# Kernel optimization log

Measured on AMD Instinct MI355X. Metric: run time of the kernel, lower is better.

The kernel has to match this reference:

```python
import jax, jax.numpy as jnp
import numpy as np

B, P, T, V, H, E, C = 256, 256, 32, 3433, 512, 300, 128


def _gru(x, h, W_ih, W_hh, b_ih, b_hh):
    # torch.nn.GRUCell math (bias=True default)
    gx = x @ W_ih.T + b_ih          # (B, 3H)
    gh = h @ W_hh.T + b_hh          # (B, 3H)
    xr, xz, xn = jnp.split(gx, 3, axis=-1)
    hr, hz, hn = jnp.split(gh, 3, axis=-1)
    r = jax.nn.sigmoid(xr + hr)
    z = jax.nn.sigmoid(xz + hz)
    n = jnp.tanh(xn + r * hn)
    return (1.0 - z) * n + z * h


def setup_inputs() -> dict:
    key = jax.random.key(0)
    ks = jax.random.split(key, 24)
    s = 0.02
    inp = {
        'word_embs': jax.random.normal(ks[0], (B, T, E), jnp.float32),
        't_feat': jax.random.normal(ks[1], (B, C), jnp.float32),
        'c_feats': jax.random.normal(ks[2], (B, P, C), jnp.float32),
        'num_words': T,
        # top-down unit (all Linears bias=False)
        'W_td1': jax.random.normal(ks[3], (128, H), jnp.float32) * s,
        'W_td2': jax.random.normal(ks[4], (128, C), jnp.float32) * s,
        'W_td3': jax.random.normal(ks[5], (128, E), jnp.float32) * s,
        'W_td':  jax.random.normal(ks[6], (128, 128), jnp.float32) * s,
        'W1_ih': jax.random.normal(ks[7], (3 * H, 128), jnp.float32) * s,
        'W1_hh': jax.random.normal(ks[8], (3 * H, H), jnp.float32) * s,
        'b1_ih': jax.random.normal(ks[9], (3 * H,), jnp.float32) * s,
        'b1_hh': jax.random.normal(ks[10], (3 * H,), jnp.float32) * s,
        # additive attention
        'W_feat': jax.random.normal(ks[11], (H, C), jnp.float32) * s,
        'W_hidd': jax.random.normal(ks[12], (H, H), jnp.float32) * s,
        'W_att':  jax.random.normal(ks[13], (1, H), jnp.float32) * s,
        # language unit
        'W_l1': jax.random.normal(ks[14], (128, C), jnp.float32) * s,
        'W_l2': jax.random.normal(ks[15], (128, H), jnp.float32) * s,
        'W_l':  jax.random.normal(ks[16], (128, 128), jnp.float32) * s,
        'W2_ih': jax.random.normal(ks[17], (3 * H, 128), jnp.float32) * s,
        'W2_hh': jax.random.normal(ks[18], (3 * H, H), jnp.float32) * s,
        'b2_ih': jax.random.normal(ks[19], (3 * H,), jnp.float32) * s,
        'b2_hh': jax.random.normal(ks[20], (3 * H,), jnp.float32) * s,
        # classifier (bias=True)
        'W_cls': jax.random.normal(ks[21], (V, H), jnp.float32) * s,
        'b_cls': jax.random.normal(ks[22], (V,), jnp.float32) * s,
    }
    return inp


def reference(word_embs, t_feat, c_feats, num_words,
              W_td1, W_td2, W_td3, W_td, W1_ih, W1_hh, b1_ih, b1_hh,
              W_feat, W_hidd, W_att, W_l1, W_l2, W_l,
              W2_ih, W2_hh, b2_ih, b2_hh, W_cls, b_cls):
    n_steps = num_words - 1  # python int, static
    # precompute attention key projection of proposals: (B, P, H)
    feat_proj = jnp.einsum('bpc,hc->bph', c_feats, W_feat)
    td_t = t_feat @ W_td2.T  # (B, 128), time-invariant

    def step_fn(carry, x_t):
        h1, h2 = carry
        # top-down input
        s = x_t @ W_td3.T + h2 @ W_td1.T + td_t
        s = jax.nn.relu(jnp.tanh(s) @ W_td.T)
        h1 = _gru(s, h1, W1_ih, W1_hh, b1_ih, b1_hh)
        # additive attention over proposals
        comb = jnp.tanh(feat_proj + (h1 @ W_hidd.T)[:, None, :])  # (B, P, H)
        scores = jnp.einsum('bph,h->bp', comb, W_att[0])           # (B, P)
        mask = jax.nn.softmax(scores, axis=1)                      # (B, P)
        attended = jnp.einsum('bpc,bp->bc', c_feats, mask)         # (B, C)
        # language input
        l = jnp.tanh(attended @ W_l1.T + h1 @ W_l2.T)
        l = jax.nn.relu(l @ W_l.T)
        h2 = _gru(l, h2, W2_ih, W2_hh, b2_ih, b2_hh)
        logits = h2 @ W_cls.T + b_cls                              # (B, V)
        return (h1, h2), (logits, mask)

    h0 = (jnp.zeros((word_embs.shape[0], H), word_embs.dtype),
          jnp.zeros((word_embs.shape[0], H), word_embs.dtype))
    xs = jnp.swapaxes(word_embs[:, :n_steps], 0, 1)  # (T-1, B, E)
    _, (logits, masks) = jax.lax.scan(step_fn, h0, xs)
    lang_cap = jnp.swapaxes(logits, 0, 1)            # (B, T-1, V)
    topdown_attn = jnp.transpose(masks, (1, 2, 0))   # (B, P, T-1)
    return lang_cap, topdown_attn
```

## Files before the change

kernel.cpp:

```cpp
#include <hip/hip_runtime.h>
#include <hip/hip_bf16.h>

namespace {

constexpr int kB  = 256;
constexpr int kP  = 256;
constexpr int kT  = 32;
constexpr int kNS = 31;
constexpr int kV  = 3433;
constexpr int kH  = 512;
constexpr int kE  = 300;
constexpr int kC  = 128;
constexpr int kG  = 1536;

typedef __bf16 bf16x8 __attribute__((ext_vector_type(8)));
typedef float f32x4 __attribute__((ext_vector_type(4)));

__device__ __forceinline__ float fexp2(float x) {
  float r; asm("v_exp_f32 %0, %1" : "=v"(r) : "v"(x)); return r;
}
__device__ __forceinline__ float frcp(float x) {
  float r; asm("v_rcp_f32 %0, %1" : "=v"(r) : "v"(x)); return r;
}
__device__ __forceinline__ float ftanh(float x) {
  float e = fexp2(x * 2.8853900817779268f);
  return 1.0f - 2.0f * frcp(e + 1.0f);
}
__device__ __forceinline__ float fsigm(float x) {
  return frcp(1.0f + fexp2(x * -1.4426950408889634f));
}
__device__ __forceinline__ float ptanh(float x) {
  x = fminf(3.0f, fmaxf(-3.0f, x));
  float t = x * x;
  float num = x * fmaf(t, fmaf(t, 378.0f + t, 17325.0f), 135135.0f);
  float den = fmaf(t, fmaf(t, fmaf(t, 28.0f, 3150.0f), 62370.0f), 135135.0f);
  return num * frcp(den);
}
__device__ __forceinline__ unsigned short f2bf(float f) {
  unsigned u = __float_as_uint(f);
  u += 0x7FFFu + ((u >> 16) & 1u);
  return (unsigned short)(u >> 16);
}
__device__ __forceinline__ float bf2f(unsigned short s) {
  return __uint_as_float((unsigned)s << 16);
}
__device__ __forceinline__ bf16x8 bload(const unsigned short* p) {
  union { uint4 u; bf16x8 v; } x;
  x.u = *(const uint4*)p;
  return x.v;
}

__global__ void k_transpose(const float* s0, const float* s1, const float* s2,
                            const float* s3, const float* s4, const float* s5,
                            const float* s6, const float* s7, const float* s8,
                            float* d0, float* d1, float* d2, float* d3,
                            float* d4, float* d5, float* d6, float* d7,
                            float* d8) {
  const float* src; float* dst; int R, Cd;
  switch (blockIdx.y) {
    case 0:  src = s0; dst = d0; R = 128;  Cd = 300; break;
    case 1:  src = s1; dst = d1; R = 128;  Cd = 512; break;
    case 2:  src = s2; dst = d2; R = 128;  Cd = 128; break;
    case 3:  src = s3; dst = d3; R = 128;  Cd = 128; break;
    case 4:  src = s4; dst = d4; R = 128;  Cd = 512; break;
    case 5:  src = s5; dst = d5; R = 128;  Cd = 128; break;
    case 6:  src = s6; dst = d6; R = 1536; Cd = 128; break;
    case 7:  src = s7; dst = d7; R = 1536; Cd = 128; break;
    default: src = s8; dst = d8; R = 512;  Cd = 512; break;
  }
  int n = R * Cd;
  for (int i = blockIdx.x * blockDim.x + threadIdx.x; i < n;
       i += gridDim.x * blockDim.x) {
    int k = i / R, r = i - k * R;
    dst[i] = src[r * Cd + k];
  }
}

__global__ void k_tobf16(const float* s0, const float* s1, const float* s2,
                         const float* s3, const float* s4, const float* s5,
                         const float* s6, const float* s7,
                         unsigned short* d0, unsigned short* d1,
                         unsigned short* d2, unsigned short* d3,
                         unsigned short* d4, unsigned short* d5,
                         unsigned short* d6, unsigned short* d7) {
  const float* s; unsigned short* d; int n;
  switch (blockIdx.y) {
    case 0:  s = s0; d = d0; n = kC * kC; break;
    case 1:  s = s1; d = d1; n = kH * kC; break;
    case 2:  s = s2; d = d2; n = kC * kC; break;
    case 3:  s = s3; d = d3; n = kC * kG; break;
    case 4:  s = s4; d = d4; n = kH * kH; break;
    case 5:  s = s5; d = d5; n = kH * kC; break;
    case 6:  s = s6; d = d6; n = kC * kC; break;
    default: s = s7; d = d7; n = kC * kG; break;
  }
  for (int i = blockIdx.x * blockDim.x + threadIdx.x; i < n;
       i += gridDim.x * blockDim.x)
    d[i] = f2bf(s[i]);
}

__global__ void k_split(const float* s0, const float* s1, const float* s2,
                        const float* s3,
                        unsigned short* h0, unsigned short* l0,
                        unsigned short* h1, unsigned short* l1,
                        unsigned short* h2, unsigned short* l2,
                        unsigned short* h3, unsigned short* l3) {
  const float* s; unsigned short* h; unsigned short* l; int n;
  switch (blockIdx.y) {
    case 0:  s = s0; h = h0; l = l0; n = kG * kH; break;
    case 1:  s = s1; h = h1; l = l1; n = kG * kH; break;
    case 2:  s = s2; h = h2; l = l2; n = kV * kH; break;
    default: s = s3; h = h3; l = l3; n = kH * kC; break;
  }
  for (int i = blockIdx.x * blockDim.x + threadIdx.x; i < n;
       i += gridDim.x * blockDim.x) {
    float v = s[i];
    unsigned short hb = f2bf(v);
    h[i] = hb;
    l[i] = f2bf(v - bf2f(hb));
  }
}

__global__ void k_init(const float* __restrict__ t_feat,
                       const float* __restrict__ W_td2,
                       float* __restrict__ td, float* __restrict__ h1,
                       float* __restrict__ h2,
                       unsigned short* __restrict__ h1h,
                       unsigned short* __restrict__ h1l,
                       unsigned short* __restrict__ h2h,
                       unsigned short* __restrict__ h2l) {
  int tid = blockIdx.x * 256 + threadIdx.x;
  int b = tid >> 7, c = tid & 127;
  const float* tf = t_feat + b * kC;
  const float* w  = W_td2 + c * kC;
  float acc = 0.f;
  for (int k = 0; k < kC; ++k) acc = fmaf(tf[k], w[k], acc);
  td[tid] = acc;
  for (int i = tid; i < kB * kH; i += (1 << 15)) {
    h1[i] = 0.f; h2[i] = 0.f;
    h1h[i] = 0; h1l[i] = 0; h2h[i] = 0; h2l[i] = 0;
  }
}

__global__ __launch_bounds__(256) void k_xw(
    const float* __restrict__ word_embs, const float* __restrict__ td3t,
    const float* __restrict__ td, float* __restrict__ xw) {
  __shared__ float xl[4 * 300];
  __shared__ float tdl[512];
  int t = blockIdx.y, b0 = blockIdx.x * 4, tid = threadIdx.x;
  #pragma unroll
  for (int r = 0; r < 4; ++r) {
    const float* xs = word_embs + (size_t)(b0 + r) * (kT * kE) + (size_t)t * kE;
    for (int e = tid; e < kE; e += 256) xl[r * kE + e] = xs[e];
  }
  for (int i = tid; i < 512; i += 256) tdl[i] = td[(size_t)b0 * kC + i];
  __syncthreads();
  #pragma unroll
  for (int q = 0; q < 2; ++q) {
    int idx = tid + q * 256;
    int r = idx >> 7, c = idx & 127;
    float acc = tdl[idx];
    const float* xr = xl + r * kE;
    const float* w3 = td3t + c;
    for (int e = 0; e < kE; ++e) acc = fmaf(xr[e], w3[(size_t)e * 128], acc);
    xw[((size_t)t * kB + b0 + r) * kC + c] = acc;
  }
}

__global__ __launch_bounds__(256) void k_prestep(
    const float* __restrict__ xw, const unsigned short* __restrict__ tdbt,
    const unsigned short* __restrict__ iht1b, const float* __restrict__ b1_ih,
    float* __restrict__ gx1) {
  __shared__ float s1l[128];
  __shared__ float s2l[128];
  __shared__ float part[256];
  int b = blockIdx.x, tid = threadIdx.x;
  if (tid < 128) s1l[tid] = ftanh(xw[(size_t)b * kC + tid]);
  __syncthreads();
  {
    int c = tid & 127, g = tid >> 7;
    float s = 0.f;
    const unsigned short* w = tdbt + (size_t)(g * 64) * kC + c;
    for (int k = 0; k < 64; ++k)
      s = fmaf(s1l[g * 64 + k], bf2f(w[(size_t)k * kC]), s);
    part[g * 128 + c] = s;
  }
  __syncthreads();
  if (tid < 128) s2l[tid] = fmaxf(part[tid] + part[128 + tid], 0.f);
  __syncthreads();
  #pragma unroll
  for (int q = 0; q < 6; ++q) {
    int j = q * 256 + tid;
    float acc = b1_ih[j];
    const unsigned short* w = iht1b + j;
    for (int k = 0; k < kC; ++k)
      acc = fmaf(s2l[k], bf2f(w[(size_t)k * kG]), acc);
    gx1[(size_t)b * kG + j] = acc;
  }
}

__device__ __forceinline__ void mm_tile_lds(
    const unsigned short* __restrict__ Ah, const unsigned short* __restrict__ Al,
    const unsigned short* __restrict__ Bh, const unsigned short* __restrict__ Bl,
    int m0, int n0, int K, int nMax, f32x4 acc[4][4],
    unsigned short* sAh, unsigned short* sAl,
    unsigned short* sBh, unsigned short* sBl) {
  int tid = threadIdx.x;
  int lane = tid & 63, wid = tid >> 6;
  int wm = (wid >> 1) * 64, wn = (wid & 1) * 64;
  int r16 = lane & 15, kq = lane >> 4;
  int rA = tid >> 2, cA = (tid & 3) * 8;
  int brow0 = n0 + rA;       if (brow0 > nMax) brow0 = nMax;
  int brow1 = n0 + rA + 64;  if (brow1 > nMax) brow1 = nMax;
  for (int k0 = 0; k0 < K; k0 += 32) {
    uint4 va0 = *(const uint4*)(Ah + (size_t)(m0 + rA) * K + k0 + cA);
    uint4 va1 = *(const uint4*)(Ah + (size_t)(m0 + rA + 64) * K + k0 + cA);
    uint4 vb0 = *(const uint4*)(Al + (size_t)(m0 + rA) * K + k0 + cA);
    uint4 vb1 = *(const uint4*)(Al + (size_t)(m0 + rA + 64) * K + k0 + cA);
    uint4 vc0 = *(const uint4*)(Bh + (size_t)brow0 * K + k0 + cA);
    uint4 vc1 = *(const uint4*)(Bh + (size_t)brow1 * K + k0 + cA);
    uint4 vd0 = *(const uint4*)(Bl + (size_t)brow0 * K + k0 + cA);
    uint4 vd1 = *(const uint4*)(Bl + (size_t)brow1 * K + k0 + cA);
    __syncthreads();
    *(uint4*)&sAh[rA * 32 + cA] = va0;
    *(uint4*)&sAh[(rA + 64) * 32 + cA] = va1;
    *(uint4*)&sAl[rA * 32 + cA] = vb0;
    *(uint4*)&sAl[(rA + 64) * 32 + cA] = vb1;
    *(uint4*)&sBh[rA * 32 + cA] = vc0;
    *(uint4*)&sBh[(rA + 64) * 32 + cA] = vc1;
    *(uint4*)&sBl[rA * 32 + cA] = vd0;
    *(uint4*)&sBl[(rA + 64) * 32 + cA] = vd1;
    __syncthreads();
    bf16x8 ah[4], al[4], bh[4], bl[4];
    #pragma unroll
    for (int i = 0; i < 4; ++i) {
      int ar = (wm + i * 16 + r16) * 32 + kq * 8;
      int br = (wn + i * 16 + r16) * 32 + kq * 8;
      ah[i] = *(const bf16x8*)&sAh[ar];
      al[i] = *(const bf16x8*)&sAl[ar];
      bh[i] = *(const bf16x8*)&sBh[br];
      bl[i] = *(const bf16x8*)&sBl[br];
    }
    #pragma unroll
    for (int i = 0; i < 4; ++i)
      #pragma unroll
      for (int j = 0; j < 4; ++j) {
        acc[i][j] = __builtin_amdgcn_mfma_f32_16x16x32_bf16(ah[i], bh[j], acc[i][j], 0, 0, 0);
        acc[i][j] = __builtin_amdgcn_mfma_f32_16x16x32_bf16(ah[i], bl[j], acc[i][j], 0, 0, 0);
        acc[i][j] = __builtin_amdgcn_mfma_f32_16x16x32_bf16(al[i], bh[j], acc[i][j], 0, 0, 0);
      }
  }
}

__global__ __launch_bounds__(256) void k_featproj(
    const float* __restrict__ A, const unsigned short* __restrict__ Wh,
    const unsigned short* __restrict__ Wl, unsigned short* __restrict__ out) {
  int lane = threadIdx.x & 63, wid = threadIdx.x >> 6;
  int wm = (wid >> 1) * 64, wn = (wid & 1) * 64;
  int r16 = lane & 15, kq = lane >> 4;
  int m0 = blockIdx.x * 128, n0 = blockIdx.y * 128;
  f32x4 acc[4][4];
  #pragma unroll
  for (int i = 0; i < 4; ++i)
    #pragma unroll
    for (int j = 0; j < 4; ++j) acc[i][j] = (f32x4){0.f, 0.f, 0.f, 0.f};
  for (int k0 = 0; k0 < kC; k0 += 32) {
    int kk = k0 + kq * 8;
    bf16x8 ah[4], al[4], bh[4], bl[4];
    #pragma unroll
    for (int i = 0; i < 4; ++i) {
      const float* pa = A + (size_t)(m0 + wm + i * 16 + r16) * kC + kk;
      float4 v0 = *(const float4*)pa;
      float4 v1 = *(const float4*)(pa + 4);
      float vv[8] = {v0.x, v0.y, v0.z, v0.w, v1.x, v1.y, v1.z, v1.w};
      union { unsigned short s[8]; bf16x8 v; } uh, ul;
      #pragma unroll
      for (int q = 0; q < 8; ++q) {
        unsigned short hb = f2bf(vv[q]);
        uh.s[q] = hb;
        ul.s[q] = f2bf(vv[q] - bf2f(hb));
      }
      ah[i] = uh.v; al[i] = ul.v;
      const unsigned short* pb = Wh + (size_t)(n0 + wn + i * 16 + r16) * kC + kk;
      const unsigned short* pl = Wl + (size_t)(n0 + wn + i * 16 + r16) * kC + kk;
      bh[i] = bload(pb); bl[i] = bload(pl);
    }
    #pragma unroll
    for (int i = 0; i < 4; ++i)
      #pragma unroll
      for (int j = 0; j < 4; ++j) {
        acc[i][j] = __builtin_amdgcn_mfma_f32_16x16x32_bf16(ah[i], bh[j], acc[i][j], 0, 0, 0);
        acc[i][j] = __builtin_amdgcn_mfma_f32_16x16x32_bf16(ah[i], bl[j], acc[i][j], 0, 0, 0);
        acc[i][j] = __builtin_amdgcn_mfma_f32_16x16x32_bf16(al[i], bh[j], acc[i][j], 0, 0, 0);
      }
  }
  #pragma unroll
  for (int i = 0; i < 4; ++i)
    #pragma unroll
    for (int j = 0; j < 4; ++j)
      #pragma unroll
      for (int r = 0; r < 4; ++r) {
        int m = m0 + wm + i * 16 + kq * 4 + r;
        int n = n0 + wn + j * 16 + r16;
        out[(size_t)m * kH + n] = f2bf(acc[i][j][r]);
      }
}

__global__ __launch_bounds__(256) void k_gh(
    const unsigned short* __restrict__ h1h, const unsigned short* __restrict__ h1l,
    const unsigned short* __restrict__ h2h, const unsigned short* __restrict__ h2l,
    const unsigned short* __restrict__ w1hh_h, const unsigned short* __restrict__ w1hh_l,
    const unsigned short* __restrict__ w2hh_h, const unsigned short* __restrict__ w2hh_l,
    const float* __restrict__ b1_hh, const float* __restrict__ b2_hh,
    float* __restrict__ gh1, float* __restrict__ gh2) {
  __shared__ __align__(16) unsigned short sAh[4096], sAl[4096], sBh[4096], sBl[4096];
  int g = blockIdx.x;
  const unsigned short *Ah, *Al, *Wh, *Wl; const float* bias; float* out;
  if (g < 24) { Ah = h1h; Al = h1l; Wh = w1hh_h; Wl = w1hh_l;
                bias = b1_hh; out = gh1; }
  else { g -= 24; Ah = h2h; Al = h2l; Wh = w2hh_h; Wl = w2hh_l;
         bias = b2_hh; out = gh2; }
  int m0 = (g / 12) * 128, n0 = (g % 12) * 128;
  f32x4 acc[4][4];
  #pragma unroll
  for (int i = 0; i < 4; ++i)
    #pragma unroll
    for (int j = 0; j < 4; ++j) acc[i][j] = (f32x4){0.f, 0.f, 0.f, 0.f};
  mm_tile_lds(Ah, Al, Wh, Wl, m0, n0, kH, kG - 1, acc, sAh, sAl, sBh, sBl);
  int tid = threadIdx.x;
  int lane = tid & 63, wid = tid >> 6;
  int wm = (wid >> 1) * 64, wn = (wid & 1) * 64;
  int r16 = lane & 15, kq = lane >> 4;
  #pragma unroll
  for (int i = 0; i < 4; ++i)
    #pragma unroll
    for (int j = 0; j < 4; ++j)
      #pragma unroll
      for (int r = 0; r < 4; ++r) {
        int m = m0 + wm + i * 16 + kq * 4 + r;
        int n = n0 + wn + j * 16 + r16;
        out[(size_t)m * kG + n] = acc[i][j][r] + bias[n];
      }
}

__global__ __launch_bounds__(1024, 4) void k_step2(
    float* __restrict__ gx1, const float* __restrict__ gh1,
    const float* __restrict__ gh2,
    float* __restrict__ h1, float* __restrict__ h2,
    unsigned short* __restrict__ h1h, unsigned short* __restrict__ h1l,
    unsigned short* __restrict__ h2h, unsigned short* __restrict__ h2l,
    const unsigned short* __restrict__ whdbT, const float* __restrict__ W_att,
    const unsigned short* __restrict__ fp, const float* __restrict__ c_feats,
    const unsigned short* __restrict__ l1bt, const unsigned short* __restrict__ l2bt,
    const unsigned short* __restrict__ lbt, const unsigned short* __restrict__ iht2b,
    const float* __restrict__ b2_ih,
    const unsigned short* __restrict__ td1bt, const unsigned short* __restrict__ tdbt,
    const unsigned short* __restrict__ iht1b, const float* __restrict__ b1_ih,
    const float* __restrict__ xw,
    unsigned short* __restrict__ h2all_h, unsigned short* __restrict__ h2all_l,
    float* __restrict__ mask_ws, int t) {
  __shared__ float partbuf[8192];
  __shared__ float h1p[512];
  __shared__ float h2p[512];
  __shared__ float hqs[512];
  __shared__ float scs[256];
  __shared__ float red[16];
  __shared__ float red2[16];
  __shared__ float attl[128];
  __shared__ float lt1[128];
  __shared__ float llv[128];
  __shared__ float s1l[128];
  __shared__ float s2l[128];
  __shared__ float gx2l[1536];
  const int b = blockIdx.x;
  const int tid = threadIdx.x;
  const int lane = tid & 63, wv = tid >> 6;

  if (tid < 512) {
    int c = tid;
    float gr = gx1[(size_t)b * kG + c];
    float gz = gx1[(size_t)b * kG + 512 + c];
    float gn = gx1[(size_t)b * kG + 1024 + c];
    float hr = gh1[(size_t)b * kG + c];
    float hz = gh1[(size_t)b * kG + 512 + c];
    float hnv = gh1[(size_t)b * kG + 1024 + c];
    float rr = fsigm(gr + hr);
    float zz = fsigm(gz + hz);
    float nn = ftanh(gn + rr * hnv);
    float ho = h1[(size_t)b * kH + c];
    float hn = (1.f - zz) * nn + zz * ho;
    h1[(size_t)b * kH + c] = hn;
    h1p[c] = hn;
    unsigned short hb = f2bf(hn);
    h1h[(size_t)b * kH + c] = hb;
    h1l[(size_t)b * kH + c] = f2bf(hn - bf2f(hb));
  }
  __syncthreads();

  {
    int cg = tid & 63, kg = tid >> 6;
    int c0 = cg * 8;
    const unsigned short* w = whdbT + (size_t)(kg * 32) * kH + c0;
    float acc[8] = {};
    #pragma unroll 4
    for (int k = 0; k < 32; ++k) {
      union { uint4 u; unsigned short s[8]; } wu;
      wu.u = *(const uint4*)(w + (size_t)k * kH);
      float h = h1p[kg * 32 + k];
      #pragma unroll
      for (int j = 0; j < 8; ++j) acc[j] = fmaf(h, bf2f(wu.s[j]), acc[j]);
    }
    float* pp = &partbuf[kg * 512 + c0];
    #pragma unroll
    for (int j = 0; j < 8; ++j) pp[j] = acc[j];
  }
  __syncthreads();
  if (tid < 512) {
    float s = 0.f;
    #pragma unroll
    for (int g = 0; g < 16; ++g) s += partbuf[g * 512 + tid];
    hqs[tid] = s;
  }
  __syncthreads();

  {
    float hq8[8], aw[8];
    #pragma unroll
    for (int j = 0; j < 8; ++j) hq8[j] = hqs[lane * 8 + j];
    {
      float4 a0 = *(const float4*)(W_att + lane * 8);
      float4 a1 = *(const float4*)(W_att + lane * 8 + 4);
      aw[0] = a0.x; aw[1] = a0.y; aw[2] = a0.z; aw[3] = a0.w;
      aw[4] = a1.x; aw[5] = a1.y; aw[6] = a1.z; aw[7] = a1.w;
    }
    const unsigned short* fpb = fp + (size_t)b * kP * kH;
    int p0 = wv * 16;
    uint4 rv = *(const uint4*)(fpb + (size_t)p0 * kH + lane * 8);
    for (int p = p0; p < p0 + 16; ++p) {
      union { uint4 v; unsigned short s[8]; } u; u.v = rv;
      if (p + 1 < p0 + 16)
        rv = *(const uint4*)(fpb + (size_t)(p + 1) * kH + lane * 8);
      float sc = 0.f;
      #pragma unroll
      for (int j = 0; j < 8; ++j) {
        float f = __uint_as_float((unsigned)u.s[j] << 16);
        sc += aw[j] * ptanh(f + hq8[j]);
      }
      #pragma unroll
      for (int m = 32; m; m >>= 1) sc += __shfl_xor(sc, m, 64);
      if (lane == 0) scs[p] = sc;
    }
  }
  __syncthreads();

  {
    float sv = (tid < 256) ? scs[tid] : -1e30f;
    float mx = sv;
    #pragma unroll
    for (int m = 32; m; m >>= 1) mx = fmaxf(mx, __shfl_xor(mx, m, 64));
    if (lane == 0) red[wv] = mx;
    __syncthreads();
    float bm = red[0];
    #pragma unroll
    for (int i = 1; i < 16; ++i) bm = fmaxf(bm, red[i]);
    float ev = (tid < 256) ? fexp2((sv - bm) * 1.4426950408889634f) : 0.f;
    float sm = ev;
    #pragma unroll
    for (int m = 32; m; m >>= 1) sm += __shfl_xor(sm, m, 64);
    if (lane == 0) red2[wv] = sm;
    __syncthreads();
    float tot = 0.f;
    #pragma unroll
    for (int i = 0; i < 16; ++i) tot += red2[i];
    if (tid < 256) {
      float mk = ev * frcp(tot);
      scs[tid] = mk;
      mask_ws[(size_t)t * (kB * kP) + (size_t)b * kP + tid] = mk;
    }
  }
  __syncthreads();

  {
    int c = tid & 127, q = tid >> 7;
    const float* cf = c_feats + ((size_t)b * kP + q * 32) * kC + c;
    const float* ms = scs + q * 32;
    float acc = 0.f;
    for (int p = 0; p < 32; ++p) acc = fmaf(ms[p], cf[(size_t)p * kC], acc);
    partbuf[q * 128 + c] = acc;
  }
  __syncthreads();
  if (tid < 128) {
    float s = 0.f;
    #pragma unroll
    for (int q = 0; q < 8; ++q) s += partbuf[q * 128 + tid];
    attl[tid] = s;
  }
  __syncthreads();

  {
    if (tid < 512) {
      int cg = tid & 15, kg = tid >> 4;
      int c0 = cg * 8;
      const unsigned short* w = l2bt + (size_t)(kg * 16) * kC + c0;
      float acc[8] = {};
      for (int k = 0; k < 16; ++k) {
        union { uint4 u; unsigned short s[8]; } wu;
        wu.u = *(const uint4*)(w + (size_t)k * kC);
        float h = h1p[kg * 16 + k];
        #pragma unroll
        for (int j = 0; j < 8; ++j) acc[j] = fmaf(h, bf2f(wu.s[j]), acc[j]);
      }
      float* pp = &partbuf[kg * 128 + c0];
      #pragma unroll
      for (int j = 0; j < 8; ++j) pp[j] = acc[j];
    } else if (tid < 768) {
      int tt = tid - 512;
      int cg = tt & 15, kg = tt >> 4;
      int c0 = cg * 8;
      const unsigned short* w = l1bt + (size_t)(kg * 8) * kC + c0;
      float acc[8] = {};
      for (int k = 0; k < 8; ++k) {
        union { uint4 u; unsigned short s[8]; } wu;
        wu.u = *(const uint4*)(w + (size_t)k * kC);
        float a = attl[kg * 8 + k];
        #pragma unroll
        for (int j = 0; j < 8; ++j) acc[j] = fmaf(a, bf2f(wu.s[j]), acc[j]);
      }
      float* pp = &partbuf[4096 + kg * 128 + c0];
      #pragma unroll
      for (int j = 0; j < 8; ++j) pp[j] = acc[j];
    }
  }
  __syncthreads();
  if (tid < 128) {
    float s = 0.f;
    #pragma unroll
    for (int g = 0; g < 32; ++g) s += partbuf[g * 128 + tid];
    #pragma unroll
    for (int g = 0; g < 16; ++g) s += partbuf[4096 + g * 128 + tid];
    lt1[tid] = ftanh(s);
  }
  __syncthreads();

  if (tid < 256) {
    int cg = tid & 15, kg = tid >> 4;
    int c0 = cg * 8;
    const unsigned short* w = lbt + (size_t)(kg * 8) * kC + c0;
    float acc[8] = {};
    for (int k = 0; k < 8; ++k) {
      union { uint4 u; unsigned short s[8]; } wu;
      wu.u = *(const uint4*)(w + (size_t)k * kC);
      float l = lt1[kg * 8 + k];
      #pragma unroll
      for (int j = 0; j < 8; ++j) acc[j] = fmaf(l, bf2f(wu.s[j]), acc[j]);
    }
    float* pp = &partbuf[kg * 128 + c0];
    #pragma unroll
    for (int j = 0; j < 8; ++j) pp[j] = acc[j];
  }
  __syncthreads();
  if (tid < 128) {
    float s = 0.f;
    #pragma unroll
    for (int g = 0; g < 16; ++g) s += partbuf[g * 128 + tid];
    llv[tid] = fmaxf(s, 0.f);
  }
  __syncthreads();

  if (tid < 768) {
    int cg = tid % 192, kg = tid / 192;
    int c0 = cg * 8;
    const unsigned short* w = iht2b + (size_t)(kg * 32) * kG + c0;
    float acc[8] = {};
    #pragma unroll 4
    for (int k = 0; k < 32; ++k) {
      union { uint4 u; unsigned short s[8]; } wu;
      wu.u = *(const uint4*)(w + (size_t)k * kG);
      float l = llv[kg * 32 + k];
      #pragma unroll
      for (int j = 0; j < 8; ++j) acc[j] = fmaf(l, bf2f(wu.s[j]), acc[j]);
    }
    float* pp = &partbuf[kg * 1536 + c0];
    #pragma unroll
    for (int j = 0; j < 8; ++j) pp[j] = acc[j];
  }
  __syncthreads();
  for (int c = tid; c < kG; c += 1024) {
    float s = b2_ih[c];
    #pragma unroll
    for (int g = 0; g < 4; ++g) s += partbuf[g * 1536 + c];
    gx2l[c] = s;
  }
  __syncthreads();
  if (tid < 512) {
    int c = tid;
    float ghr = gh2[(size_t)b * kG + c];
    float ghz = gh2[(size_t)b * kG + 512 + c];
    float ghn = gh2[(size_t)b * kG + 1024 + c];
    float rr = fsigm(gx2l[c] + ghr);
    float zz = fsigm(gx2l[512 + c] + ghz);
    float nn = ftanh(gx2l[1024 + c] + rr * ghn);
    float ho = h2[(size_t)b * kH + c];
    float hn = (1.f - zz) * nn + zz * ho;
    h2[(size_t)b * kH + c] = hn;
    h2p[c] = hn;
    unsigned short hb = f2bf(hn);
    unsigned short lb = f2bf(hn - bf2f(hb));
    h2h[(size_t)b * kH + c] = hb;
    h2l[(size_t)b * kH + c] = lb;
    size_t o = ((size_t)t * kB + b) * kH + c;
    h2all_h[o] = hb;
    h2all_l[o] = lb;
  }
  __syncthreads();

  if (t + 1 < kNS) {
    if (tid < 512) {
      int cg = tid & 15, kg = tid >> 4;
      int c0 = cg * 8;
      const unsigned short* w = td1bt + (size_t)(kg * 16) * kC + c0;
      float acc[8] = {};
      for (int k = 0; k < 16; ++k) {
        union { uint4 u; unsigned short s[8]; } wu;
        wu.u = *(const uint4*)(w + (size_t)k * kC);
        float h = h2p[kg * 16 + k];
        #pragma unroll
        for (int j = 0; j < 8; ++j) acc[j] = fmaf(h, bf2f(wu.s[j]), acc[j]);
      }
      float* pp = &partbuf[kg * 128 + c0];
      #pragma unroll
      for (int j = 0; j < 8; ++j) pp[j] = acc[j];
    }
    __syncthreads();
    if (tid < 128) {
      float s = xw[((size_t)(t + 1) * kB + b) * kC + tid];
      #pragma unroll
      for (int g = 0; g < 32; ++g) s += partbuf[g * 128 + tid];
      s1l[tid] = ftanh(s);
    }
    __syncthreads();
    if (tid < 256) {
      int cg = tid & 15, kg = tid >> 4;
      int c0 = cg * 8;
      const unsigned short* w = tdbt + (size_t)(kg * 8) * kC + c0;
      float acc[8] = {};
      for (int k = 0; k < 8; ++k) {
        union { uint4 u; unsigned short s[8]; } wu;
        wu.u = *(const uint4*)(w + (size_t)k * kC);
        float sv = s1l[kg * 8 + k];
        #pragma unroll
        for (int j = 0; j < 8; ++j) acc[j] = fmaf(sv, bf2f(wu.s[j]), acc[j]);
      }
      float* pp = &partbuf[kg * 128 + c0];
      #pragma unroll
      for (int j = 0; j < 8; ++j) pp[j] = acc[j];
    }
    __syncthreads();
    if (tid < 128) {
      float s = 0.f;
      #pragma unroll
      for (int g = 0; g < 16; ++g) s += partbuf[g * 128 + tid];
      s2l[tid] = fmaxf(s, 0.f);
    }
    __syncthreads();
    if (tid < 768) {
      int cg = tid % 192, kg = tid / 192;
      int c0 = cg * 8;
      const unsigned short* w = iht1b + (size_t)(kg * 32) * kG + c0;
      float acc[8] = {};
      #pragma unroll 4
      for (int k = 0; k < 32; ++k) {
        union { uint4 u; unsigned short s[8]; } wu;
        wu.u = *(const uint4*)(w + (size_t)k * kG);
        float sv = s2l[kg * 32 + k];
        #pragma unroll
        for (int j = 0; j < 8; ++j) acc[j] = fmaf(sv, bf2f(wu.s[j]), acc[j]);
      }
      float* pp = &partbuf[kg * 1536 + c0];
      #pragma unroll
      for (int j = 0; j < 8; ++j) pp[j] = acc[j];
    }
    __syncthreads();
    for (int c = tid; c < kG; c += 1024) {
      float s = b1_ih[c];
      #pragma unroll
      for (int g = 0; g < 4; ++g) s += partbuf[g * 1536 + c];
      gx1[(size_t)b * kG + c] = s;
    }
  }
}

__global__ __launch_bounds__(256) void k_atrans(
    const float* __restrict__ mws, float* __restrict__ attn_out) {
  int pair = blockIdx.x * 256 + threadIdx.x;
  #pragma unroll
  for (int t = 0; t < kNS; ++t)
    attn_out[(size_t)pair * kNS + t] = mws[(size_t)t * (kB * kP) + pair];
}

__global__ __launch_bounds__(256) void k_cls(
    const unsigned short* __restrict__ Ah, const unsigned short* __restrict__ Al,
    const unsigned short* __restrict__ Wh, const unsigned short* __restrict__ Wl,
    const float* __restrict__ bc, float* __restrict__ out) {
  __shared__ __align__(16) unsigned short sAh[4096], sAl[4096], sBh[4096], sBl[4096];
  int m0 = blockIdx.x * 128, n0 = blockIdx.y * 128;
  f32x4 acc[4][4];
  #pragma unroll
  for (int i = 0; i < 4; ++i)
    #pragma unroll
    for (int j = 0; j < 4; ++j) acc[i][j] = (f32x4){0.f, 0.f, 0.f, 0.f};
  mm_tile_lds(Ah, Al, Wh, Wl, m0, n0, kH, kV - 1, acc, sAh, sAl, sBh, sBl);
  int lane = threadIdx.x & 63, wid = threadIdx.x >> 6;
  int wm = (wid >> 1) * 64, wn = (wid & 1) * 64;
  int r16 = lane & 15, kq = lane >> 4;
  #pragma unroll
  for (int i = 0; i < 4; ++i)
    #pragma unroll
    for (int j = 0; j < 4; ++j)
      #pragma unroll
      for (int r = 0; r < 4; ++r) {
        int m = m0 + wm + i * 16 + kq * 4 + r;
        int n = n0 + wn + j * 16 + r16;
        if (n < kV) {
          int tt = m >> 8, b = m & 255;
          out[(size_t)b * (kNS * kV) + (size_t)tt * kV + n] = acc[i][j][r] + bc[n];
        }
      }
}

}

extern "C" void kernel_launch(void* const* d_in, const int* in_sizes, int n_in,
                              void* d_out, int out_size, void* d_ws,
                              size_t ws_size, hipStream_t stream) {
  (void)in_sizes; (void)n_in; (void)out_size; (void)ws_size;
  const float* word_embs = (const float*)d_in[0];
  const float* t_feat    = (const float*)d_in[1];
  const float* c_feats   = (const float*)d_in[2];
  const float* W_td1 = (const float*)d_in[4];
  const float* W_td2 = (const float*)d_in[5];
  const float* W_td3 = (const float*)d_in[6];
  const float* W_td  = (const float*)d_in[7];
  const float* W1_ih = (const float*)d_in[8];
  const float* W1_hh = (const float*)d_in[9];
  const float* b1_ih = (const float*)d_in[10];
  const float* b1_hh = (const float*)d_in[11];
  const float* W_feat = (const float*)d_in[12];
  const float* W_hidd = (const float*)d_in[13];
  const float* W_att  = (const float*)d_in[14];
  const float* W_l1 = (const float*)d_in[15];
  const float* W_l2 = (const float*)d_in[16];
  const float* W_l  = (const float*)d_in[17];
  const float* W2_ih = (const float*)d_in[18];
  const float* W2_hh = (const float*)d_in[19];
  const float* b2_ih = (const float*)d_in[20];
  const float* b2_hh = (const float*)d_in[21];
  const float* W_cls = (const float*)d_in[22];
  const float* b_cls = (const float*)d_in[23];

  float* lang = (float*)d_out;
  float* attn_out = lang + (size_t)kB * kNS * kV;
  unsigned short* fp = (unsigned short*)d_out;

  float* p = (float*)d_ws;
  float* h1 = p;      p += kB * kH;
  float* h2 = p;      p += kB * kH;
  float* td = p;      p += kB * kC;
  float* gx1 = p;     p += (size_t)kB * kG;
  float* gh1 = p;     p += (size_t)kB * kG;
  float* gh2 = p;     p += (size_t)kB * kG;
  float* mask_ws = p; p += (size_t)kNS * kB * kP;
  float* xw = p;      p += (size_t)kNS * kB * kC;
  float* td3t = p;    p += kE * 128;
  float* td1t = p;    p += kH * 128;
  float* tdt  = p;    p += 128 * 128;
  float* l1t  = p;    p += 128 * 128;
  float* l2t  = p;    p += kH * 128;
  float* lt   = p;    p += 128 * 128;
  float* iht1 = p;    p += 128 * kG;
  float* iht2 = p;    p += 128 * kG;
  float* whd_t = p;   p += kH * kH;

  unsigned short* u = (unsigned short*)p;
  unsigned short* h1h = u;     u += kB * kH;
  unsigned short* h1l = u;     u += kB * kH;
  unsigned short* h2h = u;     u += kB * kH;
  unsigned short* h2l = u;     u += kB * kH;
  unsigned short* w1hh_h = u;  u += (size_t)kG * kH;
  unsigned short* w1hh_l = u;  u += (size_t)kG * kH;
  unsigned short* w2hh_h = u;  u += (size_t)kG * kH;
  unsigned short* w2hh_l = u;  u += (size_t)kG * kH;
  unsigned short* wc_h = u;    u += (size_t)kV * kH;
  unsigned short* wc_l = u;    u += (size_t)kV * kH;
  unsigned short* wf_h = u;    u += (size_t)kH * kC;
  unsigned short* wf_l = u;    u += (size_t)kH * kC;
  unsigned short* h2all_h = u; u += (size_t)kNS * kB * kH;
  unsigned short* h2all_l = u; u += (size_t)kNS * kB * kH;
  unsigned short* l1bt = u;    u += kC * kC;
  unsigned short* l2bt = u;    u += (size_t)kH * kC;
  unsigned short* lbt = u;     u += kC * kC;
  unsigned short* iht2b = u;   u += (size_t)kC * kG;
  unsigned short* whdbT = u;   u += (size_t)kH * kH;
  unsigned short* td1bt = u;   u += (size_t)kH * kC;
  unsigned short* tdbt = u;    u += kC * kC;
  unsigned short* iht1b = u;   u += (size_t)kC * kG;

  k_transpose<<<dim3(64, 9), 256, 0, stream>>>(
      W_td3, W_td1, W_td, W_l1, W_l2, W_l, W1_ih, W2_ih, W_hidd,
      td3t, td1t, tdt, l1t, l2t, lt, iht1, iht2, whd_t);
  k_tobf16<<<dim3(96, 8), 256, 0, stream>>>(
      l1t, l2t, lt, iht2, whd_t, td1t, tdt, iht1,
      l1bt, l2bt, lbt, iht2b, whdbT, td1bt, tdbt, iht1b);
  k_split<<<dim3(256, 4), 256, 0, stream>>>(
      W1_hh, W2_hh, W_cls, W_feat,
      w1hh_h, w1hh_l, w2hh_h, w2hh_l, wc_h, wc_l, wf_h, wf_l);
  k_init<<<128, 256, 0, stream>>>(t_feat, W_td2, td, h1, h2,
                                  h1h, h1l, h2h, h2l);
  k_featproj<<<dim3(512, 4), 256, 0, stream>>>(c_feats, wf_h, wf_l, fp);
  k_xw<<<dim3(64, kNS), 256, 0, stream>>>(word_embs, td3t, td, xw);
  k_prestep<<<256, 256, 0, stream>>>(xw, tdbt, iht1b, b1_ih, gx1);

  for (int t = 0; t < kNS; ++t) {
    k_gh<<<48, 256, 0, stream>>>(h1h, h1l, h2h, h2l,
                                 w1hh_h, w1hh_l, w2hh_h, w2hh_l,
                                 b1_hh, b2_hh, gh1, gh2);
    k_step2<<<256, 1024, 0, stream>>>(gx1, gh1, gh2, h1, h2,
                                      h1h, h1l, h2h, h2l, whdbT, W_att, fp,
                                      c_feats, l1bt, l2bt, lbt, iht2b, b2_ih,
                                      td1bt, tdbt, iht1b, b1_ih, xw,
                                      h2all_h, h2all_l, mask_ws, t);
  }
  k_atrans<<<256, 256, 0, stream>>>(mask_ws, attn_out);
  k_cls<<<dim3(62, 27), 256, 0, stream>>>(h2all_h, h2all_l, wc_h, wc_l,
                                          b_cls, lang);
}
```

Baseline: 2.264 ms.

## Split-K recurrent GEMM, pad LDS rows, tile attention transpose, use exp tanh

The per-step hidden GEMM is split along K into two halves, which doubles the block count from 48 to 96 to fill more CUs. The step kernel sums the two partial outputs, and only the first half adds the bias. The LDS row stride is padded from 32 to 40 elements to reduce bank conflicts in both k_gh and the classifier GEMM. The final attention transpose now goes through a shared-memory tile so the writes are coalesced. The rational tanh approximation in the attention scores is replaced by the exp-based tanh, which changes numerics and cost slightly.

```diff
diff --git a/kernel.cpp b/kernel.cpp
--- a/kernel.cpp
+++ b/kernel.cpp
@@ -12,6 +12,7 @@
 constexpr int kE  = 300;
 constexpr int kC  = 128;
 constexpr int kG  = 1536;
+constexpr int kLdsStride = 40;
 
 typedef __bf16 bf16x8 __attribute__((ext_vector_type(8)));
 typedef float f32x4 __attribute__((ext_vector_type(4)));
@@ -28,13 +29,6 @@
 }
 __device__ __forceinline__ float fsigm(float x) {
   return frcp(1.0f + fexp2(x * -1.4426950408889634f));
-}
-__device__ __forceinline__ float ptanh(float x) {
-  x = fminf(3.0f, fmaxf(-3.0f, x));
-  float t = x * x;
-  float num = x * fmaf(t, fmaf(t, 378.0f + t, 17325.0f), 135135.0f);
-  float den = fmaf(t, fmaf(t, fmaf(t, 28.0f, 3150.0f), 62370.0f), 135135.0f);
-  return num * frcp(den);
 }
 __device__ __forceinline__ unsigned short f2bf(float f) {
   unsigned u = __float_as_uint(f);
@@ -202,7 +196,7 @@
 __device__ __forceinline__ void mm_tile_lds(
     const unsigned short* __restrict__ Ah, const unsigned short* __restrict__ Al,
     const unsigned short* __restrict__ Bh, const unsigned short* __restrict__ Bl,
-    int m0, int n0, int K, int nMax, f32x4 acc[4][4],
+    int m0, int n0, int K, int kbeg, int kend, int nMax, f32x4 acc[4][4],
     unsigned short* sAh, unsigned short* sAl,
     unsigned short* sBh, unsigned short* sBl) {
   int tid = threadIdx.x;
@@ -212,7 +206,7 @@
   int rA = tid >> 2, cA = (tid & 3) * 8;
   int brow0 = n0 + rA;       if (brow0 > nMax) brow0 = nMax;
   int brow1 = n0 + rA + 64;  if (brow1 > nMax) brow1 = nMax;
-  for (int k0 = 0; k0 < K; k0 += 32) {
+  for (int k0 = kbeg; k0 < kend; k0 += 32) {
     uint4 va0 = *(const uint4*)(Ah + (size_t)(m0 + rA) * K + k0 + cA);
     uint4 va1 = *(const uint4*)(Ah + (size_t)(m0 + rA + 64) * K + k0 + cA);
     uint4 vb0 = *(const uint4*)(Al + (size_t)(m0 + rA) * K + k0 + cA);
@@ -222,20 +216,20 @@
     uint4 vd0 = *(const uint4*)(Bl + (size_t)brow0 * K + k0 + cA);
     uint4 vd1 = *(const uint4*)(Bl + (size_t)brow1 * K + k0 + cA);
     __syncthreads();
-    *(uint4*)&sAh[rA * 32 + cA] = va0;
-    *(uint4*)&sAh[(rA + 64) * 32 + cA] = va1;
-    *(uint4*)&sAl[rA * 32 + cA] = vb0;
-    *(uint4*)&sAl[(rA + 64) * 32 + cA] = vb1;
-    *(uint4*)&sBh[rA * 32 + cA] = vc0;
-    *(uint4*)&sBh[(rA + 64) * 32 + cA] = vc1;
-    *(uint4*)&sBl[rA * 32 + cA] = vd0;
-    *(uint4*)&sBl[(rA + 64) * 32 + cA] = vd1;
+    *(uint4*)&sAh[rA * kLdsStride + cA] = va0;
+    *(uint4*)&sAh[(rA + 64) * kLdsStride + cA] = va1;
+    *(uint4*)&sAl[rA * kLdsStride + cA] = vb0;
+    *(uint4*)&sAl[(rA + 64) * kLdsStride + cA] = vb1;
+    *(uint4*)&sBh[rA * kLdsStride + cA] = vc0;
+    *(uint4*)&sBh[(rA + 64) * kLdsStride + cA] = vc1;
+    *(uint4*)&sBl[rA * kLdsStride + cA] = vd0;
+    *(uint4*)&sBl[(rA + 64) * kLdsStride + cA] = vd1;
     __syncthreads();
     bf16x8 ah[4], al[4], bh[4], bl[4];
     #pragma unroll
     for (int i = 0; i < 4; ++i) {
-      int ar = (wm + i * 16 + r16) * 32 + kq * 8;
-      int br = (wn + i * 16 + r16) * 32 + kq * 8;
+      int ar = (wm + i * 16 + r16) * kLdsStride + kq * 8;
+      int br = (wn + i * 16 + r16) * kLdsStride + kq * 8;
       ah[i] = *(const bf16x8*)&sAh[ar];
       al[i] = *(const bf16x8*)&sAl[ar];
       bh[i] = *(const bf16x8*)&sBh[br];
@@ -313,20 +307,26 @@
     const unsigned short* __restrict__ w2hh_h, const unsigned short* __restrict__ w2hh_l,
     const float* __restrict__ b1_hh, const float* __restrict__ b2_hh,
     float* __restrict__ gh1, float* __restrict__ gh2) {
-  __shared__ __align__(16) unsigned short sAh[4096], sAl[4096], sBh[4096], sBl[4096];
-  int g = blockIdx.x;
+  __shared__ __align__(16) unsigned short sAh[128 * kLdsStride];
+  __shared__ __align__(16) unsigned short sAl[128 * kLdsStride];
+  __shared__ __align__(16) unsigned short sBh[128 * kLdsStride];
+  __shared__ __align__(16) unsigned short sBl[128 * kLdsStride];
+  int g2 = blockIdx.x;
+  int half = g2 & 1, g = g2 >> 1;
   const unsigned short *Ah, *Al, *Wh, *Wl; const float* bias; float* out;
   if (g < 24) { Ah = h1h; Al = h1l; Wh = w1hh_h; Wl = w1hh_l;
                 bias = b1_hh; out = gh1; }
   else { g -= 24; Ah = h2h; Al = h2l; Wh = w2hh_h; Wl = w2hh_l;
          bias = b2_hh; out = gh2; }
+  out += (size_t)half * (kB * kG);
   int m0 = (g / 12) * 128, n0 = (g % 12) * 128;
   f32x4 acc[4][4];
   #pragma unroll
   for (int i = 0; i < 4; ++i)
     #pragma unroll
     for (int j = 0; j < 4; ++j) acc[i][j] = (f32x4){0.f, 0.f, 0.f, 0.f};
-  mm_tile_lds(Ah, Al, Wh, Wl, m0, n0, kH, kG - 1, acc, sAh, sAl, sBh, sBl);
+  mm_tile_lds(Ah, Al, Wh, Wl, m0, n0, kH, half * 256, half * 256 + 256,
+              kG - 1, acc, sAh, sAl, sBh, sBl);
   int tid = threadIdx.x;
   int lane = tid & 63, wid = tid >> 6;
   int wm = (wid >> 1) * 64, wn = (wid & 1) * 64;
@@ -339,7 +339,9 @@
       for (int r = 0; r < 4; ++r) {
         int m = m0 + wm + i * 16 + kq * 4 + r;
         int n = n0 + wn + j * 16 + r16;
-        out[(size_t)m * kG + n] = acc[i][j][r] + bias[n];
+        float v = acc[i][j][r];
+        if (half == 0) v += bias[n];
+        out[(size_t)m * kG + n] = v;
       }
 }
 
@@ -375,15 +377,16 @@
   const int b = blockIdx.x;
   const int tid = threadIdx.x;
   const int lane = tid & 63, wv = tid >> 6;
+  const size_t GPART = (size_t)kB * kG;
 
   if (tid < 512) {
     int c = tid;
     float gr = gx1[(size_t)b * kG + c];
     float gz = gx1[(size_t)b * kG + 512 + c];
     float gn = gx1[(size_t)b * kG + 1024 + c];
-    float hr = gh1[(size_t)b * kG + c];
-    float hz = gh1[(size_t)b * kG + 512 + c];
-    float hnv = gh1[(size_t)b * kG + 1024 + c];
+    float hr = gh1[(size_t)b * kG + c] + gh1[GPART + (size_t)b * kG + c];
+    float hz = gh1[(size_t)b * kG + 512 + c] + gh1[GPART + (size_t)b * kG + 512 + c];
+    float hnv = gh1[(size_t)b * kG + 1024 + c] + gh1[GPART + (size_t)b * kG + 1024 + c];
     float rr = fsigm(gr + hr);
     float zz = fsigm(gz + hz);
     float nn = ftanh(gn + rr * hnv);
@@ -444,7 +447,7 @@
       #pragma unroll
       for (int j = 0; j < 8; ++j) {
         float f = __uint_as_float((unsigned)u.s[j] << 16);
-        sc += aw[j] * ptanh(f + hq8[j]);
+        sc += aw[j] * ftanh(f + hq8[j]);
       }
       #pragma unroll
       for (int m = 32; m; m >>= 1) sc += __shfl_xor(sc, m, 64);
@@ -594,9 +597,9 @@
   __syncthreads();
   if (tid < 512) {
     int c = tid;
-    float ghr = gh2[(size_t)b * kG + c];
-    float ghz = gh2[(size_t)b * kG + 512 + c];
-    float ghn = gh2[(size_t)b * kG + 1024 + c];
+    float ghr = gh2[(size_t)b * kG + c] + gh2[GPART + (size_t)b * kG + c];
+    float ghz = gh2[(size_t)b * kG + 512 + c] + gh2[GPART + (size_t)b * kG + 512 + c];
+    float ghn = gh2[(size_t)b * kG + 1024 + c] + gh2[GPART + (size_t)b * kG + 1024 + c];
     float rr = fsigm(gx2l[c] + ghr);
     float zz = fsigm(gx2l[512 + c] + ghz);
     float nn = ftanh(gx2l[1024 + c] + rr * ghn);
@@ -692,24 +695,38 @@
 
 __global__ __launch_bounds__(256) void k_atrans(
     const float* __restrict__ mws, float* __restrict__ attn_out) {
-  int pair = blockIdx.x * 256 + threadIdx.x;
+  __shared__ float tile[256][33];
+  int pair0 = blockIdx.x * 256;
+  int tid = threadIdx.x;
   #pragma unroll
   for (int t = 0; t < kNS; ++t)
-    attn_out[(size_t)pair * kNS + t] = mws[(size_t)t * (kB * kP) + pair];
+    tile[tid][t] = mws[(size_t)t * (kB * kP) + pair0 + tid];
+  __syncthreads();
+  float* outb = attn_out + (size_t)pair0 * kNS;
+  #pragma unroll
+  for (int i = 0; i < kNS; ++i) {
+    int g = i * 256 + tid;
+    int pr = g / 31, tt = g - pr * 31;
+    outb[g] = tile[pr][tt];
+  }
 }
 
 __global__ __launch_bounds__(256) void k_cls(
     const unsigned short* __restrict__ Ah, const unsigned short* __restrict__ Al,
     const unsigned short* __restrict__ Wh, const unsigned short* __restrict__ Wl,
     const float* __restrict__ bc, float* __restrict__ out) {
-  __shared__ __align__(16) unsigned short sAh[4096], sAl[4096], sBh[4096], sBl[4096];
+  __shared__ __align__(16) unsigned short sAh[128 * kLdsStride];
+  __shared__ __align__(16) unsigned short sAl[128 * kLdsStride];
+  __shared__ __align__(16) unsigned short sBh[128 * kLdsStride];
+  __shared__ __align__(16) unsigned short sBl[128 * kLdsStride];
   int m0 = blockIdx.x * 128, n0 = blockIdx.y * 128;
   f32x4 acc[4][4];
   #pragma unroll
   for (int i = 0; i < 4; ++i)
     #pragma unroll
     for (int j = 0; j < 4; ++j) acc[i][j] = (f32x4){0.f, 0.f, 0.f, 0.f};
-  mm_tile_lds(Ah, Al, Wh, Wl, m0, n0, kH, kV - 1, acc, sAh, sAl, sBh, sBl);
+  mm_tile_lds(Ah, Al, Wh, Wl, m0, n0, kH, 0, kH, kV - 1, acc,
+              sAh, sAl, sBh, sBl);
   int lane = threadIdx.x & 63, wid = threadIdx.x >> 6;
   int wm = (wid >> 1) * 64, wn = (wid & 1) * 64;
   int r16 = lane & 15, kq = lane >> 4;
@@ -767,8 +784,8 @@
   float* h2 = p;      p += kB * kH;
   float* td = p;      p += kB * kC;
   float* gx1 = p;     p += (size_t)kB * kG;
-  float* gh1 = p;     p += (size_t)kB * kG;
-  float* gh2 = p;     p += (size_t)kB * kG;
+  float* gh1 = p;     p += (size_t)2 * kB * kG;
+  float* gh2 = p;     p += (size_t)2 * kB * kG;
   float* mask_ws = p; p += (size_t)kNS * kB * kP;
   float* xw = p;      p += (size_t)kNS * kB * kC;
   float* td3t = p;    p += kE * 128;
@@ -821,7 +838,7 @@
   k_prestep<<<256, 256, 0, stream>>>(xw, tdbt, iht1b, b1_ih, gx1);
 
   for (int t = 0; t < kNS; ++t) {
-    k_gh<<<48, 256, 0, stream>>>(h1h, h1l, h2h, h2l,
+    k_gh<<<96, 256, 0, stream>>>(h1h, h1l, h2h, h2l,
                                  w1hh_h, w1hh_l, w2hh_h, w2hh_l,
                                  b1_hh, b2_hh, gh1, gh2);
     k_step2<<<256, 1024, 0, stream>>>(gx1, gh1, gh2, h1, h2,
```

Measured after the change: 2.226 ms, median of 2. No clear change (-1.7%).
